# Performance work log

Measured on AMD Instinct MI355X. Metric: run time of the kernel, lower is better.

## Reference

```python
import jax, jax.numpy as jnp
import numpy as np
import math


def setup_inputs() -> dict:
    key = jax.random.key(0)
    k1, k2, k3 = jax.random.split(key, 3)
    shape = (2, 16, 2048, 64)  # (b, h, s, d)
    Q = jax.random.normal(k1, shape, dtype=jnp.float32)
    K = jax.random.normal(k2, shape, dtype=jnp.float32)
    V = jax.random.normal(k3, shape, dtype=jnp.float32)
    return {"Q": Q, "K": K, "V": V}


def reference(Q, K, V):
    b, h, s, d = Q.shape
    scale = jnp.float16(1.0 / math.sqrt(d))
    # Faithful to the torch module: fp16 QK^T and PV matmuls, fp32 softmax.
    Qh = Q.astype(jnp.float16)
    Kh = K.astype(jnp.float16)
    Vh = V.astype(jnp.float16)
    # [b,h,s,s] scores in fp16 (materialized, as in the original baddbmm)
    scores = jnp.einsum('bhsd,bhtd->bhst', Qh, Kh) * scale
    attn = jax.nn.softmax(scores.astype(jnp.float32), axis=-1).astype(jnp.float16)
    out = jnp.einsum('bhst,bhtd->bhsd', attn, Vh)
    return out.astype(jnp.float32)
```

## Files before the change

### kernel.cpp

```cpp
#include <hip/hip_runtime.h>
#include <stdint.h>

typedef _Float16 half8 __attribute__((ext_vector_type(8)));
typedef _Float16 half4 __attribute__((ext_vector_type(4)));
typedef __fp16 fp16x2 __attribute__((ext_vector_type(2)));
typedef float f32x4 __attribute__((ext_vector_type(4)));
typedef float float4v __attribute__((ext_vector_type(4)));

#define S_LEN 2048
#define D_DIM 64
#define QBLK 128
#define KVBLK 64
#define NT (S_LEN / KVBLK)
#define NBH 32
#define QSCALE 0.18033688f
#define KSTR 72

#if __has_builtin(__builtin_amdgcn_exp2f)
#define EXP2(x) __builtin_amdgcn_exp2f(x)
#else
#define EXP2(x) exp2f(x)
#endif
#define MAX3(a, b, c) fmaxf(fmaxf((a), (b)), (c))

static __device__ __forceinline__ void glds16(const void* g, void* l) {
  __builtin_amdgcn_global_load_lds(
      (__attribute__((address_space(1))) void*)(g),
      (__attribute__((address_space(3))) void*)(l), 16, 0, 0);
}
#define SBAR() do { asm volatile("" ::: "memory"); __builtin_amdgcn_s_barrier(); asm volatile("" ::: "memory"); } while (0)

__global__ __launch_bounds__(256)
void cvt_pack(const float* __restrict__ Kg, const float* __restrict__ Vg,
              _Float16* __restrict__ Kw, _Float16* __restrict__ Vw) {
  const int id = (int)(blockIdx.x * 256 + threadIdx.x);
  const int tensor = id >> 19;
  const int cid = id & 0x7FFFF;
  const int bht = cid >> 9;
  const int bh = bht >> 5, t = bht & 31;
  const int loc = cid & 511;
  const int a = loc >> 3;
  const int s = loc & 7;
  size_t srcoff;
  if (tensor == 0) {
    const int r = a;
    srcoff = (size_t)bh * (S_LEN * D_DIM) + (size_t)(t * 64 + r) * D_DIM + 8 * (s ^ (r & 7));
  } else {
    const int TI = a, c2 = s;
    const int it = TI & 3;
    const int vgi = ((TI >> 3) & 3) | (((TI >> 2) & 1) << 2) | (((TI >> 5) & 1) << 3);
    const int kq = c2 >> 1, d8 = (c2 & 1) * 8;
    srcoff = (size_t)bh * (S_LEN * D_DIM) + (size_t)(t * 64 + 4 * vgi + kq) * D_DIM + it * 16 + d8;
  }
  const float* src = (tensor ? Vg : Kg) + srcoff;
  float4v x = *(const float4v*)src;
  float4v y = *(const float4v*)(src + 4);
  half8 h = { (_Float16)x[0], (_Float16)x[1], (_Float16)x[2], (_Float16)x[3],
              (_Float16)y[0], (_Float16)y[1], (_Float16)y[2], (_Float16)y[3] };
  _Float16* dst = (tensor ? Vw : Kw) + (size_t)bht * 4096 + (size_t)loc * 8;
  *(half8*)dst = h;
}

static __device__ __forceinline__ void softmax_pack(f32x4 (&s)[4], float& m_run,
                                                    f32x4& l_acc, f32x4 (&o)[4],
                                                    half8 (&pb)[2]) {
  float plm;
  {
    float a0 = MAX3(s[0][0], s[0][1], s[0][2]);
    float a1 = MAX3(s[0][3], s[1][0], s[1][1]);
    float a2 = MAX3(s[1][2], s[1][3], s[2][0]);
    float a3 = MAX3(s[2][1], s[2][2], s[2][3]);
    float a4 = MAX3(s[3][0], s[3][1], s[3][2]);
    plm = fmaxf(MAX3(a0, a1, a2), MAX3(a3, a4, s[3][3]));
  }
  float p[16];
  if (__any(plm > m_run + 8.f)) {
    float pmax = fmaxf(plm, __shfl_xor(plm, 16, 64));
    pmax = fmaxf(pmax, __shfl_xor(pmax, 32, 64));
    const float mnew  = fmaxf(m_run, pmax);
    const float alpha = EXP2(m_run - mnew);
    m_run = mnew;
#pragma unroll
    for (int i = 0; i < 16; ++i)
      p[i] = EXP2(s[i >> 2][i & 3] - mnew);
    l_acc[0] *= alpha;
#pragma unroll
    for (int dt = 0; dt < 4; ++dt) {
      o[dt][0] *= alpha; o[dt][1] *= alpha;
      o[dt][2] *= alpha; o[dt][3] *= alpha;
    }
  } else {
#pragma unroll
    for (int i = 0; i < 16; ++i)
      p[i] = EXP2(s[i >> 2][i & 3] - m_run);
  }
#pragma unroll
  for (int kc = 0; kc < 2; ++kc) {
    fp16x2 x0 = __builtin_amdgcn_cvt_pkrtz(p[8 * kc + 0], p[8 * kc + 1]);
    fp16x2 x1 = __builtin_amdgcn_cvt_pkrtz(p[8 * kc + 2], p[8 * kc + 3]);
    fp16x2 x2 = __builtin_amdgcn_cvt_pkrtz(p[8 * kc + 4], p[8 * kc + 5]);
    fp16x2 x3 = __builtin_amdgcn_cvt_pkrtz(p[8 * kc + 6], p[8 * kc + 7]);
    half8 pk = { (_Float16)x0[0], (_Float16)x0[1], (_Float16)x1[0], (_Float16)x1[1],
                 (_Float16)x2[0], (_Float16)x2[1], (_Float16)x3[0], (_Float16)x3[1] };
    pb[kc] = pk;
  }
}

__global__ __launch_bounds__(256, 2)
void fa_fwd2(const float* __restrict__ Qg, const _Float16* __restrict__ Kw,
             const _Float16* __restrict__ Vw, float* __restrict__ Og) {
  __shared__ __attribute__((aligned(128))) _Float16 Klds[4][4096];
  __shared__ __attribute__((aligned(128))) _Float16 Vlds[4][4096];

  const int tid  = (int)threadIdx.x;
  const int wid  = tid >> 6;
  const int lane = tid & 63;
  const int g    = lane >> 4;
  const int c    = lane & 15;

  const int qtile = (int)blockIdx.x;
  const int bh    = (int)blockIdx.y;
  const size_t base = (size_t)bh * (S_LEN * D_DIM);

  const int qrowA = qtile * QBLK + wid * 16 + c;
  const int qrowB = qrowA + 64;
  half8 qfA[2], qfB[2];
#pragma unroll
  for (int kt = 0; kt < 2; ++kt) {
    const float* qpA = Qg + base + (size_t)qrowA * D_DIM + kt * 32 + 8 * g;
    const float* qpB = Qg + base + (size_t)qrowB * D_DIM + kt * 32 + 8 * g;
    float4v a0 = *(const float4v*)qpA;
    float4v a1 = *(const float4v*)(qpA + 4);
    float4v b0 = *(const float4v*)qpB;
    float4v b1 = *(const float4v*)(qpB + 4);
    half8 qa = { (_Float16)(a0[0] * QSCALE), (_Float16)(a0[1] * QSCALE),
                 (_Float16)(a0[2] * QSCALE), (_Float16)(a0[3] * QSCALE),
                 (_Float16)(a1[0] * QSCALE), (_Float16)(a1[1] * QSCALE),
                 (_Float16)(a1[2] * QSCALE), (_Float16)(a1[3] * QSCALE) };
    half8 qb = { (_Float16)(b0[0] * QSCALE), (_Float16)(b0[1] * QSCALE),
                 (_Float16)(b0[2] * QSCALE), (_Float16)(b0[3] * QSCALE),
                 (_Float16)(b1[0] * QSCALE), (_Float16)(b1[1] * QSCALE),
                 (_Float16)(b1[2] * QSCALE), (_Float16)(b1[3] * QSCALE) };
    qfA[kt] = qa; qfB[kt] = qb;
  }

  const f32x4 zero4 = {0.f, 0.f, 0.f, 0.f};
  f32x4 o_accA[4], o_accB[4];
#pragma unroll
  for (int i = 0; i < 4; ++i) { o_accA[i] = zero4; o_accB[i] = zero4; }
  f32x4 l_accA = zero4, l_accB = zero4;
  const half8 ones8 = { (_Float16)1.f, (_Float16)1.f, (_Float16)1.f, (_Float16)1.f,
                        (_Float16)1.f, (_Float16)1.f, (_Float16)1.f, (_Float16)1.f };
  float m_runA = -1.0e30f, m_runB = -1.0e30f;

  const char* kbase = (const char*)Kw + ((size_t)(bh * NT) << 13);
  const char* vbase = (const char*)Vw + ((size_t)(bh * NT) << 13);
  const int woff = wid * 2048 + lane * 16;

#define STAGE(b, t) do { \
    const char* ks_ = kbase + ((size_t)(t) << 13) + woff; \
    const char* vs_ = vbase + ((size_t)(t) << 13) + woff; \
    glds16(ks_,        &Klds[(b)][wid * 1024]); \
    glds16(ks_ + 1024, &Klds[(b)][wid * 1024 + 512]); \
    glds16(vs_,        &Vlds[(b)][wid * 1024]); \
    glds16(vs_ + 1024, &Vlds[(b)][wid * 1024 + 512]); \
  } while (0)

  const uint32_t vtb0 = (uint32_t)(uintptr_t)(&Vlds[0][0]) + 1024u * (uint32_t)g + 8u * (uint32_t)c;

  half4 vr0[16], vr1[16];
  half8 pbA0[2], pbB0[2], pbA1[2], pbB1[2];

#define TRRD_SET(VR, vt) do { \
    asm volatile("ds_read_b64_tr_b16 %0, %1 offset:0"    : "=v"(VR[0])  : "v"(vt)); \
    asm volatile("ds_read_b64_tr_b16 %0, %1 offset:128"  : "=v"(VR[1])  : "v"(vt)); \
    asm volatile("ds_read_b64_tr_b16 %0, %1 offset:256"  : "=v"(VR[2])  : "v"(vt)); \
    asm volatile("ds_read_b64_tr_b16 %0, %1 offset:384"  : "=v"(VR[3])  : "v"(vt)); \
    asm volatile("ds_read_b64_tr_b16 %0, %1 offset:512"  : "=v"(VR[4])  : "v"(vt)); \
    asm volatile("ds_read_b64_tr_b16 %0, %1 offset:640"  : "=v"(VR[5])  : "v"(vt)); \
    asm volatile("ds_read_b64_tr_b16 %0, %1 offset:768"  : "=v"(VR[6])  : "v"(vt)); \
    asm volatile("ds_read_b64_tr_b16 %0, %1 offset:896"  : "=v"(VR[7])  : "v"(vt)); \
    asm volatile("ds_read_b64_tr_b16 %0, %1 offset:4096" : "=v"(VR[8])  : "v"(vt)); \
    asm volatile("ds_read_b64_tr_b16 %0, %1 offset:4224" : "=v"(VR[9])  : "v"(vt)); \
    asm volatile("ds_read_b64_tr_b16 %0, %1 offset:4352" : "=v"(VR[10]) : "v"(vt)); \
    asm volatile("ds_read_b64_tr_b16 %0, %1 offset:4480" : "=v"(VR[11]) : "v"(vt)); \
    asm volatile("ds_read_b64_tr_b16 %0, %1 offset:4608" : "=v"(VR[12]) : "v"(vt)); \
    asm volatile("ds_read_b64_tr_b16 %0, %1 offset:4736" : "=v"(VR[13]) : "v"(vt)); \
    asm volatile("ds_read_b64_tr_b16 %0, %1 offset:4864" : "=v"(VR[14]) : "v"(vt)); \
    asm volatile("ds_read_b64_tr_b16 %0, %1 offset:4992" : "=v"(VR[15]) : "v"(vt)); \
  } while (0)

#define PV_BLOCK(VR, PBA, PBB) do { \
    __builtin_amdgcn_s_setprio(1); \
    _Pragma("unroll") \
    for (int kc = 0; kc < 2; ++kc) { \
      _Pragma("unroll") \
      for (int dt = 0; dt < 4; ++dt) { \
        half8 vf = __builtin_shufflevector(VR[kc * 8 + dt], VR[kc * 8 + 4 + dt], \
                                           0, 1, 2, 3, 4, 5, 6, 7); \
        o_accA[dt] = __builtin_amdgcn_mfma_f32_16x16x32_f16(vf, PBA[kc], o_accA[dt], 0, 0, 0); \
        o_accB[dt] = __builtin_amdgcn_mfma_f32_16x16x32_f16(vf, PBB[kc], o_accB[dt], 0, 0, 0); \
      } \
      l_accA = __builtin_amdgcn_mfma_f32_16x16x32_f16(ones8, PBA[kc], l_accA, 0, 0, 0); \
      l_accB = __builtin_amdgcn_mfma_f32_16x16x32_f16(ones8, PBB[kc], l_accB, 0, 0, 0); \
    } \
    __builtin_amdgcn_s_setprio(0); \
  } while (0)

#define ITER(T, VRC, PBAC, PBBC, DO_PV, VRP, PBAP, PBBP) do { \
    if ((T) + 2 < NT) { \
      STAGE(((T) + 2) & 3, (T) + 2); \
      asm volatile("s_waitcnt vmcnt(8)" ::: "memory"); \
    } else if ((T) + 1 < NT) { \
      asm volatile("s_waitcnt vmcnt(4)" ::: "memory"); \
    } else { \
      asm volatile("s_waitcnt vmcnt(0)" ::: "memory"); \
    } \
    __builtin_amdgcn_sched_barrier(0); \
    SBAR(); \
    const _Float16* kcur = &Klds[(T) & 3][0]; \
    const uint32_t vt = vtb0 + (uint32_t)(((T) & 3) << 13); \
    f32x4 sA[4], sB[4]; \
    _Pragma("unroll") \
    for (int ct = 0; ct < 4; ++ct) { sA[ct] = zero4; sB[ct] = zero4; } \
    __builtin_amdgcn_s_setprio(1); \
    _Pragma("unroll") \
    for (int ct = 0; ct < 4; ++ct) { \
      _Pragma("unroll") \
      for (int kt = 0; kt < 2; ++kt) { \
        half8 kb = *(half8*)&kcur[(ct * 16 + c) * 64 + (((4 * kt + g) ^ (c & 7)) << 3)]; \
        sA[ct] = __builtin_amdgcn_mfma_f32_16x16x32_f16(kb, qfA[kt], sA[ct], 0, 0, 0); \
        sB[ct] = __builtin_amdgcn_mfma_f32_16x16x32_f16(kb, qfB[kt], sB[ct], 0, 0, 0); \
      } \
    } \
    __builtin_amdgcn_s_setprio(0); \
    TRRD_SET(VRC, vt); \
    if (DO_PV) { \
      asm volatile("s_waitcnt lgkmcnt(15)" ::: "memory");  \
      __builtin_amdgcn_sched_barrier(0); \
      PV_BLOCK(VRP, PBAP, PBBP); \
    } \
    softmax_pack(sA, m_runA, l_accA, o_accA, PBAC); \
    softmax_pack(sB, m_runB, l_accB, o_accB, PBBC); \
  } while (0)

  asm volatile("s_waitcnt vmcnt(0)" ::: "memory");
  STAGE(0, 0);
  STAGE(1, 1);

  ITER(0, vr0, pbA0, pbB0, 0, vr1, pbA1, pbB1);
  for (int t = 1; t + 1 < NT; t += 2) {
    ITER(t,     vr1, pbA1, pbB1, 1, vr0, pbA0, pbB0);
    ITER(t + 1, vr0, pbA0, pbB0, 1, vr1, pbA1, pbB1);
  }
  ITER(NT - 1, vr1, pbA1, pbB1, 1, vr0, pbA0, pbB0);
  asm volatile("s_waitcnt lgkmcnt(0)" ::: "memory");
  __builtin_amdgcn_sched_barrier(0);
  PV_BLOCK(vr1, pbA1, pbB1);
#undef ITER
#undef PV_BLOCK
#undef TRRD_SET
#undef STAGE

  const float invA = 1.0f / l_accA[0];
  const float invB = 1.0f / l_accB[0];
#pragma unroll
  for (int dt = 0; dt < 4; ++dt) {
    float4v wA = { o_accA[dt][0] * invA, o_accA[dt][1] * invA,
                   o_accA[dt][2] * invA, o_accA[dt][3] * invA };
    *(float4v*)&Og[base + (size_t)qrowA * D_DIM + dt * 16 + g * 4] = wA;
    float4v wB = { o_accB[dt][0] * invB, o_accB[dt][1] * invB,
                   o_accB[dt][2] * invB, o_accB[dt][3] * invB };
    *(float4v*)&Og[base + (size_t)qrowB * D_DIM + dt * 16 + g * 4] = wB;
  }
}

__global__ __launch_bounds__(256)
void fa_fwd_fb(const float* __restrict__ Qg, const float* __restrict__ Kg,
               const float* __restrict__ Vg, float* __restrict__ Og) {
  __shared__ _Float16 Klds[KVBLK * KSTR];
  __shared__ __attribute__((aligned(128))) _Float16 Vlds[KVBLK * D_DIM];

  const int tid  = (int)threadIdx.x;
  const int wid  = tid >> 6;
  const int lane = tid & 63;
  const int g    = lane >> 4;
  const int c    = lane & 15;

  const int qtile = (int)blockIdx.x;
  const int bh    = (int)blockIdx.y;
  const size_t base = (size_t)bh * (S_LEN * D_DIM);

  const int qrow = qtile * 64 + wid * 16 + c;
  half8 qf[2];
#pragma unroll
  for (int kt = 0; kt < 2; ++kt) {
    const float* qp = Qg + base + (size_t)qrow * D_DIM + kt * 32 + 8 * g;
    float4v a = *(const float4v*)qp;
    float4v b = *(const float4v*)(qp + 4);
    half8 q;
    q[0] = (_Float16)(a[0] * QSCALE); q[1] = (_Float16)(a[1] * QSCALE);
    q[2] = (_Float16)(a[2] * QSCALE); q[3] = (_Float16)(a[3] * QSCALE);
    q[4] = (_Float16)(b[0] * QSCALE); q[5] = (_Float16)(b[1] * QSCALE);
    q[6] = (_Float16)(b[2] * QSCALE); q[7] = (_Float16)(b[3] * QSCALE);
    qf[kt] = q;
  }

  const f32x4 zero4 = {0.f, 0.f, 0.f, 0.f};
  f32x4 o_acc[4];
#pragma unroll
  for (int i = 0; i < 4; ++i) o_acc[i] = zero4;
  float m_run = -1.0e30f, l_run = 0.f;

  const int srow = tid >> 4;
  const int scol = (tid & 15) * 4;
  const int vgi = tid >> 4;
  const int vlg = tid & 15;
  const int vk  = vgi * 4 + (vlg >> 2);
  const int vsub = 8 * (vgi & 3) + 4 * ((vgi >> 2) & 1) + 32 * (vgi >> 3);
  const uint32_t vtb = (uint32_t)(uintptr_t)(&Vlds[0]) + 1024u * (uint32_t)g + 8u * (uint32_t)c;

  for (int t = 0; t < NT; ++t) {
    const int kv0 = t * KVBLK;
    __syncthreads();
#pragma unroll
    for (int rr = 0; rr < 4; ++rr) {
      const int row = srow + rr * 16;
      const float* kp = Kg + base + (size_t)(kv0 + row) * D_DIM + scol;
      float4v kx = *(const float4v*)kp;
      half4 kh = { (_Float16)kx[0], (_Float16)kx[1], (_Float16)kx[2], (_Float16)kx[3] };
      *(half4*)&Klds[row * KSTR + scol] = kh;
    }
#pragma unroll
    for (int it = 0; it < 4; ++it) {
      const int d = it * 16 + (vlg & 3) * 4;
      const float* vp = Vg + base + (size_t)(kv0 + vk) * D_DIM + d;
      float4v vx = *(const float4v*)vp;
      half4 vh = { (_Float16)vx[0], (_Float16)vx[1], (_Float16)vx[2], (_Float16)vx[3] };
      *(half4*)&Vlds[(vsub + it) * 64 + (vlg >> 2) * 16 + (vlg & 3) * 4] = vh;
    }
    __syncthreads();

    f32x4 s_acc[4];
#pragma unroll
    for (int ct = 0; ct < 4; ++ct) s_acc[ct] = zero4;
#pragma unroll
    for (int ct = 0; ct < 4; ++ct) {
#pragma unroll
      for (int kt = 0; kt < 2; ++kt) {
        half8 kb = *(half8*)&Klds[(ct * 16 + c) * KSTR + kt * 32 + 8 * g];
        s_acc[ct] = __builtin_amdgcn_mfma_f32_16x16x32_f16(kb, qf[kt], s_acc[ct], 0, 0, 0);
      }
    }

    float pmax = -1.0e30f;
#pragma unroll
    for (int ct = 0; ct < 4; ++ct)
#pragma unroll
      for (int r = 0; r < 4; ++r) pmax = fmaxf(pmax, s_acc[ct][r]);
    pmax = fmaxf(pmax, __shfl_xor(pmax, 16, 64));
    pmax = fmaxf(pmax, __shfl_xor(pmax, 32, 64));
    const float mnew  = fmaxf(m_run, pmax);
    const float alpha = exp2f(m_run - mnew);
    m_run = mnew;

    float p[16];
    float psum = 0.f;
#pragma unroll
    for (int i = 0; i < 16; ++i) {
      p[i] = exp2f(s_acc[i >> 2][i & 3] - mnew);
      psum += p[i];
    }
    psum += __shfl_xor(psum, 16, 64);
    psum += __shfl_xor(psum, 32, 64);
    l_run = l_run * alpha + psum;
#pragma unroll
    for (int dt = 0; dt < 4; ++dt) {
      o_acc[dt][0] *= alpha; o_acc[dt][1] *= alpha;
      o_acc[dt][2] *= alpha; o_acc[dt][3] *= alpha;
    }

    half8 pb[2];
#pragma unroll
    for (int kc = 0; kc < 2; ++kc) {
      fp16x2 x0 = __builtin_amdgcn_cvt_pkrtz(p[8 * kc + 0], p[8 * kc + 1]);
      fp16x2 x1 = __builtin_amdgcn_cvt_pkrtz(p[8 * kc + 2], p[8 * kc + 3]);
      fp16x2 x2 = __builtin_amdgcn_cvt_pkrtz(p[8 * kc + 4], p[8 * kc + 5]);
      fp16x2 x3 = __builtin_amdgcn_cvt_pkrtz(p[8 * kc + 6], p[8 * kc + 7]);
      half8 pk = { (_Float16)x0[0], (_Float16)x0[1], (_Float16)x1[0], (_Float16)x1[1],
                   (_Float16)x2[0], (_Float16)x2[1], (_Float16)x3[0], (_Float16)x3[1] };
      pb[kc] = pk;
    }

    half4 vr[16];
#define TRRD(i, offstr) \
    asm volatile("ds_read_b64_tr_b16 %0, %1 offset:" offstr : "=v"(vr[i]) : "v"(vtb))
    TRRD(0,  "0");    TRRD(1,  "128");  TRRD(2,  "256");  TRRD(3,  "384");
    TRRD(4,  "512");  TRRD(5,  "640");  TRRD(6,  "768");  TRRD(7,  "896");
    TRRD(8,  "4096"); TRRD(9,  "4224"); TRRD(10, "4352"); TRRD(11, "4480");
    TRRD(12, "4608"); TRRD(13, "4736"); TRRD(14, "4864"); TRRD(15, "4992");
#undef TRRD
    asm volatile("s_waitcnt lgkmcnt(0)" ::: "memory");
    __builtin_amdgcn_sched_barrier(0);

#pragma unroll
    for (int kc = 0; kc < 2; ++kc) {
#pragma unroll
      for (int dt = 0; dt < 4; ++dt) {
        half8 vf = __builtin_shufflevector(vr[kc * 8 + dt], vr[kc * 8 + 4 + dt],
                                           0, 1, 2, 3, 4, 5, 6, 7);
        o_acc[dt] = __builtin_amdgcn_mfma_f32_16x16x32_f16(vf, pb[kc], o_acc[dt], 0, 0, 0);
      }
    }
  }

  const float invl = 1.0f / l_run;
#pragma unroll
  for (int dt = 0; dt < 4; ++dt) {
    float4v w = { o_acc[dt][0] * invl, o_acc[dt][1] * invl,
                  o_acc[dt][2] * invl, o_acc[dt][3] * invl };
    *(float4v*)&Og[base + (size_t)qrow * D_DIM + dt * 16 + g * 4] = w;
  }
}

extern "C" void kernel_launch(void* const* d_in, const int* in_sizes, int n_in,
                              void* d_out, int out_size, void* d_ws, size_t ws_size,
                              hipStream_t stream) {
  const float* Q = (const float*)d_in[0];
  const float* K = (const float*)d_in[1];
  const float* V = (const float*)d_in[2];
  float* O = (float*)d_out;
  dim3 block(256);
  if (ws_size >= (size_t)16 * 1024 * 1024) {
    _Float16* Kw = (_Float16*)d_ws;
    _Float16* Vw = Kw + (size_t)NBH * S_LEN * D_DIM;
    hipLaunchKernelGGL(cvt_pack, dim3(4096), block, 0, stream, K, V, Kw, Vw);
    hipLaunchKernelGGL(fa_fwd2, dim3(S_LEN / QBLK, NBH), block, 0, stream, Q, Kw, Vw, O);
  } else {
    hipLaunchKernelGGL(fa_fwd_fb, dim3(S_LEN / 64, NBH), block, 0, stream, Q, K, V, O);
  }
}
```

Baseline: 61.74 us.

## Split KV sequence across two blocks with 512-thread tiles and merge kernel

Adds a split-KV flash attention path. Each 512-thread block (8 waves) handles 256 query rows over half of the KV tiles and writes unnormalized partial outputs plus running max and sum to workspace. A separate merge kernel then rescales and combines the two halves. Each K/V tile staged in LDS is now shared across more query rows and the split keeps the same block count as before. The cost is extra global traffic for the fp32 partial outputs, one more kernel launch, and a path that runs only when the workspace is large enough.

```diff
diff --git a/kernel.cpp b/kernel.cpp
--- a/kernel.cpp
+++ b/kernel.cpp
@@ -6,13 +6,14 @@
 typedef __fp16 fp16x2 __attribute__((ext_vector_type(2)));
 typedef float f32x4 __attribute__((ext_vector_type(4)));
 typedef float float4v __attribute__((ext_vector_type(4)));
+typedef float float2v __attribute__((ext_vector_type(2)));
 
 #define S_LEN 2048
 #define D_DIM 64
-#define QBLK 128
 #define KVBLK 64
 #define NT (S_LEN / KVBLK)
 #define NBH 32
+#define NROW (NBH * S_LEN)
 #define QSCALE 0.18033688f
 #define KSTR 72
 
@@ -106,9 +107,10 @@
   }
 }
 
-__global__ __launch_bounds__(256, 2)
-void fa_fwd2(const float* __restrict__ Qg, const _Float16* __restrict__ Kw,
-             const _Float16* __restrict__ Vw, float* __restrict__ Og) {
+__global__ __launch_bounds__(512, 2)
+void fa_fwd_split(const float* __restrict__ Qg, const _Float16* __restrict__ Kw,
+                  const _Float16* __restrict__ Vw, float* __restrict__ Op,
+                  float2v* __restrict__ mlb) {
   __shared__ __attribute__((aligned(128))) _Float16 Klds[4][4096];
   __shared__ __attribute__((aligned(128))) _Float16 Vlds[4][4096];
 
@@ -120,10 +122,12 @@
 
   const int qtile = (int)blockIdx.x;
   const int bh    = (int)blockIdx.y;
+  const int split = (int)blockIdx.z;
+  const int t0 = split * (NT / 2), t1 = t0 + (NT / 2);
   const size_t base = (size_t)bh * (S_LEN * D_DIM);
 
-  const int qrowA = qtile * QBLK + wid * 16 + c;
-  const int qrowB = qrowA + 64;
+  const int qrowA = qtile * 256 + wid * 16 + c;
+  const int qrowB = qrowA + 128;
   half8 qfA[2], qfB[2];
 #pragma unroll
   for (int kt = 0; kt < 2; ++kt) {
@@ -155,15 +159,11 @@
 
   const char* kbase = (const char*)Kw + ((size_t)(bh * NT) << 13);
   const char* vbase = (const char*)Vw + ((size_t)(bh * NT) << 13);
-  const int woff = wid * 2048 + lane * 16;
+  const int woff = tid * 16;
 
 #define STAGE(b, t) do { \
-    const char* ks_ = kbase + ((size_t)(t) << 13) + woff; \
-    const char* vs_ = vbase + ((size_t)(t) << 13) + woff; \
-    glds16(ks_,        &Klds[(b)][wid * 1024]); \
-    glds16(ks_ + 1024, &Klds[(b)][wid * 1024 + 512]); \
-    glds16(vs_,        &Vlds[(b)][wid * 1024]); \
-    glds16(vs_ + 1024, &Vlds[(b)][wid * 1024 + 512]); \
+    glds16(kbase + ((size_t)(t) << 13) + woff, &Klds[(b)][tid * 8]); \
+    glds16(vbase + ((size_t)(t) << 13) + woff, &Vlds[(b)][tid * 8]); \
   } while (0)
 
   const uint32_t vtb0 = (uint32_t)(uintptr_t)(&Vlds[0][0]) + 1024u * (uint32_t)g + 8u * (uint32_t)c;
@@ -208,6 +208,195 @@
   } while (0)
 
 #define ITER(T, VRC, PBAC, PBBC, DO_PV, VRP, PBAP, PBBP) do { \
+    if ((T) + 1 < t1) { \
+      asm volatile("s_waitcnt vmcnt(2)" ::: "memory"); \
+    } else { \
+      asm volatile("s_waitcnt vmcnt(0)" ::: "memory"); \
+    } \
+    __builtin_amdgcn_sched_barrier(0); \
+    SBAR(); \
+    if ((T) + 2 < t1) STAGE(((T) + 2) & 3, (T) + 2); \
+    const _Float16* kcur = &Klds[(T) & 3][0]; \
+    const uint32_t vt = vtb0 + (uint32_t)(((T) & 3) << 13); \
+    f32x4 sA[4], sB[4]; \
+    _Pragma("unroll") \
+    for (int ct = 0; ct < 4; ++ct) { sA[ct] = zero4; sB[ct] = zero4; } \
+    __builtin_amdgcn_s_setprio(1); \
+    _Pragma("unroll") \
+    for (int ct = 0; ct < 4; ++ct) { \
+      _Pragma("unroll") \
+      for (int kt = 0; kt < 2; ++kt) { \
+        half8 kb = *(half8*)&kcur[(ct * 16 + c) * 64 + (((4 * kt + g) ^ (c & 7)) << 3)]; \
+        sA[ct] = __builtin_amdgcn_mfma_f32_16x16x32_f16(kb, qfA[kt], sA[ct], 0, 0, 0); \
+        sB[ct] = __builtin_amdgcn_mfma_f32_16x16x32_f16(kb, qfB[kt], sB[ct], 0, 0, 0); \
+      } \
+    } \
+    __builtin_amdgcn_s_setprio(0); \
+    TRRD_SET(VRC, vt); \
+    if (DO_PV) { \
+      asm volatile("s_waitcnt lgkmcnt(15)" ::: "memory"); \
+      __builtin_amdgcn_sched_barrier(0); \
+      PV_BLOCK(VRP, PBAP, PBBP); \
+    } \
+    softmax_pack(sA, m_runA, l_accA, o_accA, PBAC); \
+    softmax_pack(sB, m_runB, l_accB, o_accB, PBBC); \
+  } while (0)
+
+  asm volatile("s_waitcnt vmcnt(0)" ::: "memory");
+  STAGE(0, t0);
+  STAGE(1, t0 + 1);
+
+  ITER(t0, vr0, pbA0, pbB0, 0, vr1, pbA1, pbB1);
+  for (int t = t0 + 1; t + 1 < t1; t += 2) {
+    ITER(t,     vr1, pbA1, pbB1, 1, vr0, pbA0, pbB0);
+    ITER(t + 1, vr0, pbA0, pbB0, 1, vr1, pbA1, pbB1);
+  }
+  ITER(t1 - 1, vr1, pbA1, pbB1, 1, vr0, pbA0, pbB0);
+  asm volatile("s_waitcnt lgkmcnt(0)" ::: "memory");
+  __builtin_amdgcn_sched_barrier(0);
+  PV_BLOCK(vr1, pbA1, pbB1);
+#undef ITER
+#undef PV_BLOCK
+#undef TRRD_SET
+#undef STAGE
+
+  float* op = Op + ((size_t)(split * NBH + bh)) * (S_LEN * D_DIM);
+#pragma unroll
+  for (int dt = 0; dt < 4; ++dt) {
+    *(float4v*)&op[(size_t)qrowA * D_DIM + dt * 16 + g * 4] = o_accA[dt];
+    *(float4v*)&op[(size_t)qrowB * D_DIM + dt * 16 + g * 4] = o_accB[dt];
+  }
+  if (g == 0) {
+    float2v* mlp = mlb + (size_t)(split * NBH + bh) * S_LEN;
+    float2v mA = { m_runA, l_accA[0] };
+    float2v mB = { m_runB, l_accB[0] };
+    mlp[qrowA] = mA;
+    mlp[qrowB] = mB;
+  }
+}
+
+__global__ __launch_bounds__(256)
+void fa_merge(const float* __restrict__ Op, const float2v* __restrict__ mlb,
+              float* __restrict__ Og) {
+  const int id = (int)(blockIdx.x * 256 + threadIdx.x);
+  const int R  = id >> 4;
+  const int cq = (id & 15) * 4;
+  float2v ml0 = mlb[R];
+  float2v ml1 = mlb[NROW + R];
+  const float ms = fmaxf(ml0[0], ml1[0]);
+  const float a0 = exp2f(ml0[0] - ms);
+  const float a1 = exp2f(ml1[0] - ms);
+  const float inv = 1.0f / (ml0[1] * a0 + ml1[1] * a1);
+  const float f0 = a0 * inv, f1 = a1 * inv;
+  float4v o0 = *(const float4v*)&Op[(size_t)R * D_DIM + cq];
+  float4v o1 = *(const float4v*)&Op[(size_t)(NROW + R) * D_DIM + cq];
+  float4v w = { o0[0] * f0 + o1[0] * f1, o0[1] * f0 + o1[1] * f1,
+                o0[2] * f0 + o1[2] * f1, o0[3] * f0 + o1[3] * f1 };
+  *(float4v*)&Og[(size_t)R * D_DIM + cq] = w;
+}
+
+__global__ __launch_bounds__(256, 2)
+void fa_fwd2(const float* __restrict__ Qg, const _Float16* __restrict__ Kw,
+             const _Float16* __restrict__ Vw, float* __restrict__ Og) {
+  __shared__ __attribute__((aligned(128))) _Float16 Klds[4][4096];
+  __shared__ __attribute__((aligned(128))) _Float16 Vlds[4][4096];
+
+  const int tid  = (int)threadIdx.x;
+  const int wid  = tid >> 6;
+  const int lane = tid & 63;
+  const int g    = lane >> 4;
+  const int c    = lane & 15;
+
+  const int qtile = (int)blockIdx.x;
+  const int bh    = (int)blockIdx.y;
+  const size_t base = (size_t)bh * (S_LEN * D_DIM);
+
+  const int qrowA = qtile * 128 + wid * 16 + c;
+  const int qrowB = qrowA + 64;
+  half8 qfA[2], qfB[2];
+#pragma unroll
+  for (int kt = 0; kt < 2; ++kt) {
+    const float* qpA = Qg + base + (size_t)qrowA * D_DIM + kt * 32 + 8 * g;
+    const float* qpB = Qg + base + (size_t)qrowB * D_DIM + kt * 32 + 8 * g;
+    float4v a0 = *(const float4v*)qpA;
+    float4v a1 = *(const float4v*)(qpA + 4);
+    float4v b0 = *(const float4v*)qpB;
+    float4v b1 = *(const float4v*)(qpB + 4);
+    half8 qa = { (_Float16)(a0[0] * QSCALE), (_Float16)(a0[1] * QSCALE),
+                 (_Float16)(a0[2] * QSCALE), (_Float16)(a0[3] * QSCALE),
+                 (_Float16)(a1[0] * QSCALE), (_Float16)(a1[1] * QSCALE),
+                 (_Float16)(a1[2] * QSCALE), (_Float16)(a1[3] * QSCALE) };
+    half8 qb = { (_Float16)(b0[0] * QSCALE), (_Float16)(b0[1] * QSCALE),
+                 (_Float16)(b0[2] * QSCALE), (_Float16)(b0[3] * QSCALE),
+                 (_Float16)(b1[0] * QSCALE), (_Float16)(b1[1] * QSCALE),
+                 (_Float16)(b1[2] * QSCALE), (_Float16)(b1[3] * QSCALE) };
+    qfA[kt] = qa; qfB[kt] = qb;
+  }
+
+  const f32x4 zero4 = {0.f, 0.f, 0.f, 0.f};
+  f32x4 o_accA[4], o_accB[4];
+#pragma unroll
+  for (int i = 0; i < 4; ++i) { o_accA[i] = zero4; o_accB[i] = zero4; }
+  f32x4 l_accA = zero4, l_accB = zero4;
+  const half8 ones8 = { (_Float16)1.f, (_Float16)1.f, (_Float16)1.f, (_Float16)1.f,
+                        (_Float16)1.f, (_Float16)1.f, (_Float16)1.f, (_Float16)1.f };
+  float m_runA = -1.0e30f, m_runB = -1.0e30f;
+
+  const char* kbase = (const char*)Kw + ((size_t)(bh * NT) << 13);
+  const char* vbase = (const char*)Vw + ((size_t)(bh * NT) << 13);
+  const int woff = wid * 2048 + lane * 16;
+
+#define STAGE(b, t) do { \
+    const char* ks_ = kbase + ((size_t)(t) << 13) + woff; \
+    const char* vs_ = vbase + ((size_t)(t) << 13) + woff; \
+    glds16(ks_,        &Klds[(b)][wid * 1024]); \
+    glds16(ks_ + 1024, &Klds[(b)][wid * 1024 + 512]); \
+    glds16(vs_,        &Vlds[(b)][wid * 1024]); \
+    glds16(vs_ + 1024, &Vlds[(b)][wid * 1024 + 512]); \
+  } while (0)
+
+  const uint32_t vtb0 = (uint32_t)(uintptr_t)(&Vlds[0][0]) + 1024u * (uint32_t)g + 8u * (uint32_t)c;
+
+  half4 vr0[16], vr1[16];
+  half8 pbA0[2], pbB0[2], pbA1[2], pbB1[2];
+
+#define TRRD_SET(VR, vt) do { \
+    asm volatile("ds_read_b64_tr_b16 %0, %1 offset:0"    : "=v"(VR[0])  : "v"(vt)); \
+    asm volatile("ds_read_b64_tr_b16 %0, %1 offset:128"  : "=v"(VR[1])  : "v"(vt)); \
+    asm volatile("ds_read_b64_tr_b16 %0, %1 offset:256"  : "=v"(VR[2])  : "v"(vt)); \
+    asm volatile("ds_read_b64_tr_b16 %0, %1 offset:384"  : "=v"(VR[3])  : "v"(vt)); \
+    asm volatile("ds_read_b64_tr_b16 %0, %1 offset:512"  : "=v"(VR[4])  : "v"(vt)); \
+    asm volatile("ds_read_b64_tr_b16 %0, %1 offset:640"  : "=v"(VR[5])  : "v"(vt)); \
+    asm volatile("ds_read_b64_tr_b16 %0, %1 offset:768"  : "=v"(VR[6])  : "v"(vt)); \
+    asm volatile("ds_read_b64_tr_b16 %0, %1 offset:896"  : "=v"(VR[7])  : "v"(vt)); \
+    asm volatile("ds_read_b64_tr_b16 %0, %1 offset:4096" : "=v"(VR[8])  : "v"(vt)); \
+    asm volatile("ds_read_b64_tr_b16 %0, %1 offset:4224" : "=v"(VR[9])  : "v"(vt)); \
+    asm volatile("ds_read_b64_tr_b16 %0, %1 offset:4352" : "=v"(VR[10]) : "v"(vt)); \
+    asm volatile("ds_read_b64_tr_b16 %0, %1 offset:4480" : "=v"(VR[11]) : "v"(vt)); \
+    asm volatile("ds_read_b64_tr_b16 %0, %1 offset:4608" : "=v"(VR[12]) : "v"(vt)); \
+    asm volatile("ds_read_b64_tr_b16 %0, %1 offset:4736" : "=v"(VR[13]) : "v"(vt)); \
+    asm volatile("ds_read_b64_tr_b16 %0, %1 offset:4864" : "=v"(VR[14]) : "v"(vt)); \
+    asm volatile("ds_read_b64_tr_b16 %0, %1 offset:4992" : "=v"(VR[15]) : "v"(vt)); \
+  } while (0)
+
+#define PV_BLOCK(VR, PBA, PBB) do { \
+    __builtin_amdgcn_s_setprio(1); \
+    _Pragma("unroll") \
+    for (int kc = 0; kc < 2; ++kc) { \
+      _Pragma("unroll") \
+      for (int dt = 0; dt < 4; ++dt) { \
+        half8 vf = __builtin_shufflevector(VR[kc * 8 + dt], VR[kc * 8 + 4 + dt], \
+                                           0, 1, 2, 3, 4, 5, 6, 7); \
+        o_accA[dt] = __builtin_amdgcn_mfma_f32_16x16x32_f16(vf, PBA[kc], o_accA[dt], 0, 0, 0); \
+        o_accB[dt] = __builtin_amdgcn_mfma_f32_16x16x32_f16(vf, PBB[kc], o_accB[dt], 0, 0, 0); \
+      } \
+      l_accA = __builtin_amdgcn_mfma_f32_16x16x32_f16(ones8, PBA[kc], l_accA, 0, 0, 0); \
+      l_accB = __builtin_amdgcn_mfma_f32_16x16x32_f16(ones8, PBB[kc], l_accB, 0, 0, 0); \
+    } \
+    __builtin_amdgcn_s_setprio(0); \
+  } while (0)
+
+#define ITER(T, VRC, PBAC, PBBC, DO_PV, VRP, PBAP, PBBP) do { \
     if ((T) + 2 < NT) { \
       STAGE(((T) + 2) & 3, (T) + 2); \
       asm volatile("s_waitcnt vmcnt(8)" ::: "memory"); \
@@ -236,7 +425,7 @@
     __builtin_amdgcn_s_setprio(0); \
     TRRD_SET(VRC, vt); \
     if (DO_PV) { \
-      asm volatile("s_waitcnt lgkmcnt(15)" ::: "memory");  \
+      asm volatile("s_waitcnt lgkmcnt(15)" ::: "memory"); \
       __builtin_amdgcn_sched_barrier(0); \
       PV_BLOCK(VRP, PBAP, PBBP); \
     } \
@@ -430,13 +619,22 @@
   const float* K = (const float*)d_in[1];
   const float* V = (const float*)d_in[2];
   float* O = (float*)d_out;
-  dim3 block(256);
-  if (ws_size >= (size_t)16 * 1024 * 1024) {
+  const size_t ws_split = 51380224u;
+  const size_t ws_pack  = (size_t)16 * 1024 * 1024;
+  if (ws_size >= ws_pack) {
     _Float16* Kw = (_Float16*)d_ws;
     _Float16* Vw = Kw + (size_t)NBH * S_LEN * D_DIM;
-    hipLaunchKernelGGL(cvt_pack, dim3(4096), block, 0, stream, K, V, Kw, Vw);
-    hipLaunchKernelGGL(fa_fwd2, dim3(S_LEN / QBLK, NBH), block, 0, stream, Q, Kw, Vw, O);
+    hipLaunchKernelGGL(cvt_pack, dim3(4096), dim3(256), 0, stream, K, V, Kw, Vw);
+    if (ws_size >= ws_split) {
+      float*   Op  = (float*)(Vw + (size_t)NBH * S_LEN * D_DIM);
+      float2v* mlb = (float2v*)(Op + (size_t)2 * NROW * D_DIM);
+      hipLaunchKernelGGL(fa_fwd_split, dim3(S_LEN / 256, NBH, 2), dim3(512), 0, stream,
+                         Q, Kw, Vw, Op, mlb);
+      hipLaunchKernelGGL(fa_merge, dim3(NROW * 16 / 256), dim3(256), 0, stream, Op, mlb, O);
+    } else {
+      hipLaunchKernelGGL(fa_fwd2, dim3(S_LEN / 128, NBH), dim3(256), 0, stream, Q, Kw, Vw, O);
+    }
   } else {
-    hipLaunchKernelGGL(fa_fwd_fb, dim3(S_LEN / 64, NBH), block, 0, stream, Q, K, V, O);
-  }
-}
+    hipLaunchKernelGGL(fa_fwd_fb, dim3(S_LEN / 64, NBH), dim3(256), 0, stream, Q, K, V, O);
+  }
+}
```

Result: slower. 78.79 us (+27.6%).
